# Kernel optimization log

Measured on AMD Instinct MI355X. Metric: run time of the kernel, lower is better.

The kernel has to match this reference:

```python
import jax, jax.numpy as jnp
import numpy as np

N_NODES = 100000
N_EDGES = 1600000
IN_DIM, HID_DIM, OUT_DIM = 128, 128, 64


def setup_inputs() -> dict:
    key = jax.random.key(0)
    k1, k2, k3, k4, k5 = jax.random.split(key, 5)
    x = jax.random.normal(k1, (N_NODES, IN_DIM), dtype=jnp.float32)
    edge_index = jax.random.randint(k2, (2, N_EDGES), 0, N_NODES, dtype=jnp.int64)
    # PyG GCNConv linear weights (no bias); Glorot-ish scale for stability
    W1 = jax.random.normal(k3, (IN_DIM, HID_DIM), dtype=jnp.float32) * 0.05
    W2 = jax.random.normal(k4, (HID_DIM, HID_DIM), dtype=jnp.float32) * 0.05
    W3 = jax.random.normal(k5, (HID_DIM, OUT_DIM), dtype=jnp.float32) * 0.05
    return {"x": x, "edge_index": edge_index, "W1": W1, "W2": W2, "W3": W3}


def _gcn_conv(h, W, src, dst, num_nodes):
    # GCNConv(add_self_loops=False, normalize=False, bias=False):
    # linear transform, then scatter-add messages from src into dst
    msg = jnp.take(h @ W, src, axis=0)          # [E, d_out] gather
    return jax.ops.segment_sum(msg, dst, num_segments=num_nodes)  # [N, d_out]


def reference(x, edge_index, W1, W2, W3):
    num_nodes = x.shape[0]
    src, dst = edge_index[0], edge_index[1]
    h = jax.nn.relu(_gcn_conv(x, W1, src, dst, num_nodes))
    # dropout p=0.0 / eval mode -> identity
    h = jax.nn.relu(_gcn_conv(h, W2, src, dst, num_nodes))
    out = _gcn_conv(h, W3, src, dst, num_nodes)
    return jax.nn.log_softmax(out, axis=1)
```

## Files before the change

kernel.cpp:

```cpp
#include <hip/hip_runtime.h>
#include <hip/hip_bf16.h>

#define KDIM 128

typedef __attribute__((ext_vector_type(8))) __bf16 bf16x8;
typedef __attribute__((ext_vector_type(4))) float f32x4;
typedef __attribute__((ext_vector_type(2))) float f32x2;

static __device__ __forceinline__ unsigned short f2bf(float f) {
  unsigned u = __float_as_uint(f);
  u += 0x7fffu + ((u >> 16) & 1u);
  return (unsigned short)(u >> 16);
}
static __device__ __forceinline__ unsigned pack_bf16x2(float a, float b) {
  return (unsigned)f2bf(a) | ((unsigned)f2bf(b) << 16);
}
static __device__ __forceinline__ unsigned relu2(unsigned u) {
  unsigned r = u;
  if (u & 0x00008000u) r &= 0xffff0000u;
  if (u & 0x80000000u) r &= 0x0000ffffu;
  return r;
}

static __device__ __forceinline__ unsigned char f2fp8(float f) {
#if __has_builtin(__builtin_amdgcn_cvt_pk_fp8_f32)
  return (unsigned char)(__builtin_amdgcn_cvt_pk_fp8_f32(f, f, 0, false) & 0xff);
#else
  unsigned s = (__float_as_uint(f) >> 24) & 0x80u;
  float a = fminf(fabsf(f), 448.f);
  if (a < 0.015625f) {
    unsigned m = (unsigned)(a * 512.f + 0.5f);
    return (unsigned char)(s | m);
  }
  unsigned v = __float_as_uint(a);
  v += 0x7ffffu + ((v >> 20) & 1u);
  unsigned em = (v >> 20) - 960u;
  if (em > 0x7eu) em = 0x7eu;
  return (unsigned char)(s | em);
#endif
}
static __device__ __forceinline__ float fp8dec(unsigned b) {
  unsigned s = (b & 0x80u) << 24;
  unsigned em = b & 0x7fu;
  float mag = (em >= 8) ? __uint_as_float((em + 960u) << 20)
                        : (float)em * 0.001953125f;
  return __uint_as_float(__float_as_uint(mag) | s);
}
static __device__ __forceinline__ float4 fp8x4_to_f32(unsigned u) {
#if __has_builtin(__builtin_amdgcn_cvt_pk_f32_fp8)
  f32x2 lo = __builtin_amdgcn_cvt_pk_f32_fp8(u, false);
  f32x2 hi = __builtin_amdgcn_cvt_pk_f32_fp8(u, true);
  return make_float4(lo[0], lo[1], hi[0], hi[1]);
#else
  return make_float4(fp8dec(u & 255u), fp8dec((u >> 8) & 255u),
                     fp8dec((u >> 16) & 255u), fp8dec(u >> 24));
#endif
}

__global__ __launch_bounds__(256) void wtrans_k(const float* __restrict__ W1,
                                                const float* __restrict__ W2,
                                                const float* __restrict__ W3,
                                                unsigned short* __restrict__ Wt) {
  const int t = blockIdx.x * 256 + threadIdx.x;
  if (t >= 40960) return;
  if (t < 16384) {
    Wt[t] = f2bf(W1[(t & 127) * 128 + (t >> 7)]);
  } else if (t < 32768) {
    const int u = t - 16384;
    Wt[t] = f2bf(W2[(u & 127) * 128 + (u >> 7)]);
  } else {
    const int u = t - 32768;
    Wt[t] = f2bf(W3[(u & 127) * 64 + (u >> 7)]);
  }
}

template<int NOUT, bool AF32, bool RELU>
__global__ __launch_bounds__(512) void gemm_mfma_k(const void* __restrict__ Av,
                                                   const unsigned short* __restrict__ Wt,
                                                   unsigned char* __restrict__ C, int M) {
  constexpr int NT = NOUT / 16;
  __shared__ unsigned short Ws[NOUT][136];

  const int tid = threadIdx.x;
  for (int i = tid; i < NOUT * 16; i += 512) {
    const int n = i >> 4, k8 = i & 15;
    const uint4 v = *reinterpret_cast<const uint4*>(&Wt[n * KDIM + k8 * 8]);
    *reinterpret_cast<uint4*>(&Ws[n][k8 * 8]) = v;
  }

  const int wv = tid >> 6;
  const int l  = tid & 63;
  const int am = l & 15;
  const int kb = l >> 4;
  const int arow_g = blockIdx.x * 128 + wv * 16 + am;
  const bool valid = arow_g < M;
  const int arow = valid ? arow_g : 0;

  uint4 afr[4];
  if constexpr (AF32) {
    const float* A = (const float*)Av;
    #pragma unroll
    for (int ks = 0; ks < 4; ++ks) {
      const float4 lo = *reinterpret_cast<const float4*>(&A[(size_t)arow * 128 + ks * 32 + kb * 8]);
      const float4 hi = *reinterpret_cast<const float4*>(&A[(size_t)arow * 128 + ks * 32 + kb * 8 + 4]);
      afr[ks] = make_uint4(pack_bf16x2(lo.x, lo.y), pack_bf16x2(lo.z, lo.w),
                           pack_bf16x2(hi.x, hi.y), pack_bf16x2(hi.z, hi.w));
    }
  } else {
    const unsigned* A = (const unsigned*)Av;
    #pragma unroll
    for (int ks = 0; ks < 4; ++ks) {
      uint4 u = *reinterpret_cast<const uint4*>(&A[(size_t)arow * 64 + ks * 16 + kb * 4]);
      if constexpr (RELU) {
        u.x = relu2(u.x); u.y = relu2(u.y); u.z = relu2(u.z); u.w = relu2(u.w);
      }
      afr[ks] = u;
    }
  }
  if (!valid) {
    afr[0] = make_uint4(0, 0, 0, 0); afr[1] = afr[0];
    afr[2] = afr[0];                 afr[3] = afr[0];
  }

  f32x4 acc[NT];
  #pragma unroll
  for (int nt = 0; nt < NT; ++nt) {
    acc[nt][0] = 0.f; acc[nt][1] = 0.f; acc[nt][2] = 0.f; acc[nt][3] = 0.f;
  }

  __syncthreads();
  #pragma unroll
  for (int ks = 0; ks < 4; ++ks) {
    const bf16x8 a = __builtin_bit_cast(bf16x8, afr[ks]);
    #pragma unroll
    for (int nt = 0; nt < NT; ++nt) {
      const uint4 bv = *reinterpret_cast<const uint4*>(&Ws[nt * 16 + am][ks * 32 + kb * 8]);
      acc[nt] = __builtin_amdgcn_mfma_f32_16x16x32_bf16(
          a, __builtin_bit_cast(bf16x8, bv), acc[nt], 0, 0, 0);
    }
  }

  const int crow0 = blockIdx.x * 128 + wv * 16 + kb * 4;
  #pragma unroll
  for (int nt = 0; nt < NT; ++nt) {
    #pragma unroll
    for (int r = 0; r < 4; ++r) {
      const int rr = crow0 + r;
      if (rr < M) C[(size_t)rr * NOUT + nt * 16 + am] = f2fp8(acc[nt][r]);
    }
  }
}

__global__ __launch_bounds__(512) void hist_k(const int* __restrict__ dst,
                                              int* __restrict__ histT,
                                              int E, int nbins) {
  __shared__ int h[512];
  for (int i = threadIdx.x; i < nbins; i += 512) h[i] = 0;
  __syncthreads();
  const int E4 = E >> 2;
  for (int i = blockIdx.x * 512 + threadIdx.x; i < E4; i += 256 * 512) {
    const int4 d4 = *reinterpret_cast<const int4*>(&dst[i * 4]);
    atomicAdd(&h[d4.x >> 8], 1);
    atomicAdd(&h[d4.y >> 8], 1);
    atomicAdd(&h[d4.z >> 8], 1);
    atomicAdd(&h[d4.w >> 8], 1);
  }
  if (blockIdx.x == 0 && threadIdx.x < (E & 3))
    atomicAdd(&h[dst[E4 * 4 + threadIdx.x] >> 8], 1);
  __syncthreads();
  for (int i = threadIdx.x; i < nbins; i += 512)
    histT[i * 256 + blockIdx.x] = h[i];
}

__global__ __launch_bounds__(256) void scan1_k(const int* __restrict__ in,
                                               int* __restrict__ out,
                                               int* __restrict__ bsum, int N) {
  __shared__ int ls[256];
  const int t = threadIdx.x;
  const int base = blockIdx.x * 2048 + t * 8;
  int v[8];
  if (base + 8 <= N) {
    *reinterpret_cast<int4*>(&v[0]) = *reinterpret_cast<const int4*>(&in[base]);
    *reinterpret_cast<int4*>(&v[4]) = *reinterpret_cast<const int4*>(&in[base + 4]);
  } else {
    #pragma unroll
    for (int j = 0; j < 8; ++j) v[j] = (base + j < N) ? in[base + j] : 0;
  }
  int s = 0;
  #pragma unroll
  for (int j = 0; j < 8; ++j) { const int tmp = v[j]; v[j] = s; s += tmp; }
  int x = s;
  ls[t] = x;
  __syncthreads();
  for (int off = 1; off < 256; off <<= 1) {
    int y = 0;
    if (t >= off) y = ls[t - off];
    __syncthreads();
    x += y;
    ls[t] = x;
    __syncthreads();
  }
  const int excl = x - s;
  #pragma unroll
  for (int j = 0; j < 8; ++j)
    if (base + j < N) out[base + j] = excl + v[j];
  if (t == 255) bsum[blockIdx.x] = x;
}

__global__ __launch_bounds__(64) void scan2_k(const int* __restrict__ bsum,
                                              int* __restrict__ bscan, int NB) {
  const int t = threadIdx.x;
  const int v = (t < NB) ? bsum[t] : 0;
  int x = v;
  #pragma unroll
  for (int off = 1; off < 64; off <<= 1) {
    const int y = __shfl_up(x, off, 64);
    if (t >= off) x += y;
  }
  bscan[t] = x - v;
}

__global__ __launch_bounds__(512) void binscatter_k(const int* __restrict__ src,
                                                    const int* __restrict__ dst,
                                                    const int* __restrict__ histOff,
                                                    const int* __restrict__ bscan,
                                                    unsigned* __restrict__ epack,
                                                    int E, int nbins) {
  __shared__ int cur[512];
  for (int i = threadIdx.x; i < nbins; i += 512) {
    const int gi = i * 256 + blockIdx.x;
    cur[i] = histOff[gi] + bscan[gi >> 11];
  }
  __syncthreads();
  const int E4 = E >> 2;
  for (int i = blockIdx.x * 512 + threadIdx.x; i < E4; i += 256 * 512) {
    const int4 d4 = *reinterpret_cast<const int4*>(&dst[i * 4]);
    const int4 s4 = *reinterpret_cast<const int4*>(&src[i * 4]);
    int p;
    p = atomicAdd(&cur[d4.x >> 8], 1); epack[p] = ((unsigned)(d4.x & 255) << 17) | (unsigned)s4.x;
    p = atomicAdd(&cur[d4.y >> 8], 1); epack[p] = ((unsigned)(d4.y & 255) << 17) | (unsigned)s4.y;
    p = atomicAdd(&cur[d4.z >> 8], 1); epack[p] = ((unsigned)(d4.z & 255) << 17) | (unsigned)s4.z;
    p = atomicAdd(&cur[d4.w >> 8], 1); epack[p] = ((unsigned)(d4.w & 255) << 17) | (unsigned)s4.w;
  }
  if (blockIdx.x == 0 && threadIdx.x < (E & 3)) {
    const int e = E4 * 4 + threadIdx.x;
    const int d = dst[e];
    const int p = atomicAdd(&cur[d >> 8], 1);
    epack[p] = ((unsigned)(d & 255) << 17) | (unsigned)src[e];
  }
}

__global__ __launch_bounds__(512) void binsort_k(const unsigned* __restrict__ epack,
                                                 const int* __restrict__ histOff,
                                                 const int* __restrict__ bscan,
                                                 int* __restrict__ rowptr,
                                                 int* __restrict__ col,
                                                 int N, int E, int nbins) {
  __shared__ int hist[256];
  __shared__ int ls[256];
  __shared__ int cur[256];
  const int b = blockIdx.x;
  const int t = threadIdx.x;
  const int i0 = b * 256;
  const int beg = histOff[i0] + bscan[i0 >> 11];
  int end = E;
  if (b + 1 < nbins) {
    const int i1 = (b + 1) * 256;
    end = histOff[i1] + bscan[i1 >> 11];
  }

  if (t < 256) hist[t] = 0;
  __syncthreads();
  for (int j = beg + t; j < end; j += 512)
    atomicAdd(&hist[epack[j] >> 17], 1);
  __syncthreads();

  int v = 0, x = 0;
  if (t < 256) { v = hist[t]; x = v; ls[t] = x; }
  __syncthreads();
  for (int off = 1; off < 256; off <<= 1) {
    int y = 0;
    if (t < 256 && t >= off) y = ls[t - off];
    __syncthreads();
    if (t < 256) { x += y; ls[t] = x; }
    __syncthreads();
  }
  if (t < 256) {
    const int excl = x - v;
    cur[t] = excl;
    const int g = b * 256 + t;
    if (g <= N) rowptr[g] = beg + excl;
  }
  if (b == nbins - 1 && t == 0) rowptr[N] = E;
  __syncthreads();
  for (int j = beg + t; j < end; j += 512) {
    const unsigned p = epack[j];
    const int pos = atomicAdd(&cur[p >> 17], 1);
    col[beg + pos] = (int)(p & 0x1ffffu);
  }
}

__global__ __launch_bounds__(256) void gather128_k(const uint2* __restrict__ H64,
                                                   const int* __restrict__ rowptr,
                                                   const int* __restrict__ col,
                                                   unsigned* __restrict__ out, int N) {
  const int w = (int)((blockIdx.x * 256u + threadIdx.x) >> 6);
  const int lane = threadIdx.x & 63;
  const int q = lane >> 4;
  const int l4 = lane & 15;
  if (w >= N) return;
  const int beg = __builtin_amdgcn_readfirstlane(rowptr[w]);
  const int end = __builtin_amdgcn_readfirstlane(rowptr[w + 1]);

  float4 a0A = make_float4(0.f, 0.f, 0.f, 0.f), a0B = make_float4(0.f, 0.f, 0.f, 0.f);
  float4 a1A = make_float4(0.f, 0.f, 0.f, 0.f), a1B = make_float4(0.f, 0.f, 0.f, 0.f);

  int e = beg;
  for (; e + 16 <= end; e += 16) {
    const int s0 = col[e + q];
    const int s1 = col[e + 4 + q];
    const int s2 = col[e + 8 + q];
    const int s3 = col[e + 12 + q];
    const uint2 u0 = H64[(size_t)s0 * 16 + l4];
    const uint2 u1 = H64[(size_t)s1 * 16 + l4];
    const uint2 u2 = H64[(size_t)s2 * 16 + l4];
    const uint2 u3 = H64[(size_t)s3 * 16 + l4];
    float4 v;
    v = fp8x4_to_f32(u0.x); a0A.x += v.x; a0A.y += v.y; a0A.z += v.z; a0A.w += v.w;
    v = fp8x4_to_f32(u0.y); a0B.x += v.x; a0B.y += v.y; a0B.z += v.z; a0B.w += v.w;
    v = fp8x4_to_f32(u1.x); a1A.x += v.x; a1A.y += v.y; a1A.z += v.z; a1A.w += v.w;
    v = fp8x4_to_f32(u1.y); a1B.x += v.x; a1B.y += v.y; a1B.z += v.z; a1B.w += v.w;
    v = fp8x4_to_f32(u2.x); a0A.x += v.x; a0A.y += v.y; a0A.z += v.z; a0A.w += v.w;
    v = fp8x4_to_f32(u2.y); a0B.x += v.x; a0B.y += v.y; a0B.z += v.z; a0B.w += v.w;
    v = fp8x4_to_f32(u3.x); a1A.x += v.x; a1A.y += v.y; a1A.z += v.z; a1A.w += v.w;
    v = fp8x4_to_f32(u3.y); a1B.x += v.x; a1B.y += v.y; a1B.z += v.z; a1B.w += v.w;
  }
  for (; e + 4 <= end; e += 4) {
    const uint2 u = H64[(size_t)col[e + q] * 16 + l4];
    float4 v;
    v = fp8x4_to_f32(u.x); a0A.x += v.x; a0A.y += v.y; a0A.z += v.z; a0A.w += v.w;
    v = fp8x4_to_f32(u.y); a0B.x += v.x; a0B.y += v.y; a0B.z += v.z; a0B.w += v.w;
  }
  if (q < end - e) {
    const uint2 u = H64[(size_t)col[e + q] * 16 + l4];
    float4 v;
    v = fp8x4_to_f32(u.x); a1A.x += v.x; a1A.y += v.y; a1A.z += v.z; a1A.w += v.w;
    v = fp8x4_to_f32(u.y); a1B.x += v.x; a1B.y += v.y; a1B.z += v.z; a1B.w += v.w;
  }

  float4 aA, aB;
  aA.x = a0A.x + a1A.x; aA.y = a0A.y + a1A.y;
  aA.z = a0A.z + a1A.z; aA.w = a0A.w + a1A.w;
  aB.x = a0B.x + a1B.x; aB.y = a0B.y + a1B.y;
  aB.z = a0B.z + a1B.z; aB.w = a0B.w + a1B.w;

  aA.x += __shfl_xor(aA.x, 16, 64); aA.x += __shfl_xor(aA.x, 32, 64);
  aA.y += __shfl_xor(aA.y, 16, 64); aA.y += __shfl_xor(aA.y, 32, 64);
  aA.z += __shfl_xor(aA.z, 16, 64); aA.z += __shfl_xor(aA.z, 32, 64);
  aA.w += __shfl_xor(aA.w, 16, 64); aA.w += __shfl_xor(aA.w, 32, 64);
  aB.x += __shfl_xor(aB.x, 16, 64); aB.x += __shfl_xor(aB.x, 32, 64);
  aB.y += __shfl_xor(aB.y, 16, 64); aB.y += __shfl_xor(aB.y, 32, 64);
  aB.z += __shfl_xor(aB.z, 16, 64); aB.z += __shfl_xor(aB.z, 32, 64);
  aB.w += __shfl_xor(aB.w, 16, 64); aB.w += __shfl_xor(aB.w, 32, 64);

  if (q == 0) {
    const uint4 pk = make_uint4(pack_bf16x2(aA.x, aA.y), pack_bf16x2(aA.z, aA.w),
                                pack_bf16x2(aB.x, aB.y), pack_bf16x2(aB.z, aB.w));
    *reinterpret_cast<uint4*>(&out[(size_t)w * 64 + l4 * 4]) = pk;
  }
}

__global__ __launch_bounds__(256) void gather64lsm_k(const unsigned* __restrict__ H32,
                                                     const int* __restrict__ rowptr,
                                                     const int* __restrict__ col,
                                                     float* __restrict__ out, int N) {
  const int w = (int)((blockIdx.x * 256u + threadIdx.x) >> 6);
  const int lane = threadIdx.x & 63;
  const int q = lane >> 4;
  const int l4 = lane & 15;
  if (w >= N) return;
  const int beg = __builtin_amdgcn_readfirstlane(rowptr[w]);
  const int end = __builtin_amdgcn_readfirstlane(rowptr[w + 1]);

  float4 acc0 = make_float4(0.f, 0.f, 0.f, 0.f);
  float4 acc1 = make_float4(0.f, 0.f, 0.f, 0.f);

  int e = beg;
  for (; e + 16 <= end; e += 16) {
    const int s0 = col[e + q];
    const int s1 = col[e + 4 + q];
    const int s2 = col[e + 8 + q];
    const int s3 = col[e + 12 + q];
    const unsigned u0 = H32[(size_t)s0 * 16 + l4];
    const unsigned u1 = H32[(size_t)s1 * 16 + l4];
    const unsigned u2 = H32[(size_t)s2 * 16 + l4];
    const unsigned u3 = H32[(size_t)s3 * 16 + l4];
    float4 v;
    v = fp8x4_to_f32(u0); acc0.x += v.x; acc0.y += v.y; acc0.z += v.z; acc0.w += v.w;
    v = fp8x4_to_f32(u1); acc1.x += v.x; acc1.y += v.y; acc1.z += v.z; acc1.w += v.w;
    v = fp8x4_to_f32(u2); acc0.x += v.x; acc0.y += v.y; acc0.z += v.z; acc0.w += v.w;
    v = fp8x4_to_f32(u3); acc1.x += v.x; acc1.y += v.y; acc1.z += v.z; acc1.w += v.w;
  }
  for (; e + 8 <= end; e += 8) {
    const int s0 = col[e + q];
    const int s1 = col[e + 4 + q];
    const float4 v0 = fp8x4_to_f32(H32[(size_t)s0 * 16 + l4]);
    const float4 v1 = fp8x4_to_f32(H32[(size_t)s1 * 16 + l4]);
    acc0.x += v0.x; acc0.y += v0.y; acc0.z += v0.z; acc0.w += v0.w;
    acc1.x += v1.x; acc1.y += v1.y; acc1.z += v1.z; acc1.w += v1.w;
  }
  if (e + 4 <= end) {
    const float4 v = fp8x4_to_f32(H32[(size_t)col[e + q] * 16 + l4]);
    acc0.x += v.x; acc0.y += v.y; acc0.z += v.z; acc0.w += v.w;
    e += 4;
  }
  if (e + q < end) {
    const float4 v = fp8x4_to_f32(H32[(size_t)col[e + q] * 16 + l4]);
    acc1.x += v.x; acc1.y += v.y; acc1.z += v.z; acc1.w += v.w;
  }

  float4 a;
  a.x = acc0.x + acc1.x;
  a.y = acc0.y + acc1.y;
  a.z = acc0.z + acc1.z;
  a.w = acc0.w + acc1.w;
  a.x += __shfl_xor(a.x, 16, 64); a.x += __shfl_xor(a.x, 32, 64);
  a.y += __shfl_xor(a.y, 16, 64); a.y += __shfl_xor(a.y, 32, 64);
  a.z += __shfl_xor(a.z, 16, 64); a.z += __shfl_xor(a.z, 32, 64);
  a.w += __shfl_xor(a.w, 16, 64); a.w += __shfl_xor(a.w, 32, 64);

  float m = fmaxf(fmaxf(a.x, a.y), fmaxf(a.z, a.w));
  #pragma unroll
  for (int o = 8; o > 0; o >>= 1) m = fmaxf(m, __shfl_xor(m, o, 64));
  float s = __expf(a.x - m) + __expf(a.y - m) + __expf(a.z - m) + __expf(a.w - m);
  #pragma unroll
  for (int o = 8; o > 0; o >>= 1) s += __shfl_xor(s, o, 64);
  const float ls = __logf(s);

  if (lane < 16) {
    *reinterpret_cast<float4*>(&out[(size_t)w * 64 + l4 * 4]) =
        make_float4(a.x - m - ls, a.y - m - ls, a.z - m - ls, a.w - m - ls);
  }
}

extern "C" void kernel_launch(void* const* d_in, const int* in_sizes, int n_in,
                              void* d_out, int out_size, void* d_ws, size_t ws_size,
                              hipStream_t stream) {
  const float* x  = (const float*)d_in[0];
  const int*   ei = (const int*)d_in[1];
  const float* W1 = (const float*)d_in[2];
  const float* W2 = (const float*)d_in[3];
  const float* W3 = (const float*)d_in[4];
  float* out = (float*)d_out;

  const int N = in_sizes[0] / KDIM;
  const int E = in_sizes[1] / 2;
  const int* src = ei;
  const int* dst = ei + E;

  const int nbins = (N + 255) / 256;
  const int ncells = nbins * 256;
  const int scan_blocks = (ncells + 2047) / 2048;

  unsigned char* H = (unsigned char*)d_ws;
  unsigned* AGGp = (unsigned*)(H + (size_t)N * 128);
  unsigned short* Wt1 = (unsigned short*)(AGGp + (size_t)N * 64);
  unsigned short* Wt2 = Wt1 + 128 * 128;
  unsigned short* Wt3 = Wt2 + 128 * 128;
  int* col     = (int*)(Wt3 + 64 * 128);
  int* rowptr  = col + E;
  int* histT   = rowptr + (N + 8);
  int* histOff = histT + 131072;
  int* bsum2   = histOff + 131072;
  int* bscan2  = bsum2 + 64;
  unsigned* epack = (unsigned*)AGGp;

  wtrans_k<<<(40960 + 255) / 256, 256, 0, stream>>>(W1, W2, W3, Wt1);

  hist_k<<<256, 512, 0, stream>>>(dst, histT, E, nbins);
  scan1_k<<<scan_blocks, 256, 0, stream>>>(histT, histOff, bsum2, ncells);
  scan2_k<<<1, 64, 0, stream>>>(bsum2, bscan2, scan_blocks);
  binscatter_k<<<256, 512, 0, stream>>>(src, dst, histOff, bscan2, epack, E, nbins);
  binsort_k<<<nbins, 512, 0, stream>>>(epack, histOff, bscan2, rowptr, col, N, E, nbins);

  const int gemm_grid = (N + 127) / 128;
  const int gather_grid = (N + 3) / 4;

  gemm_mfma_k<128, true, false><<<gemm_grid, 512, 0, stream>>>(x, Wt1, H, N);
  gather128_k<<<gather_grid, 256, 0, stream>>>((const uint2*)H, rowptr, col, AGGp, N);

  gemm_mfma_k<128, false, true><<<gemm_grid, 512, 0, stream>>>(AGGp, Wt2, H, N);
  gather128_k<<<gather_grid, 256, 0, stream>>>((const uint2*)H, rowptr, col, AGGp, N);

  gemm_mfma_k<64, false, true><<<gemm_grid, 512, 0, stream>>>(AGGp, Wt3, H, N);
  gather64lsm_k<<<gather_grid, 256, 0, stream>>>((const unsigned*)H, rowptr, col, out, N);
}
```

Measured before the change: 216.1 us.

## Merge weight transpose into histogram and run layer-1 GEMM alongside binscatter

The weight transpose/bf16 conversion is folded into the histogram kernel, with 160 threads per block covering the 40960 weight elements. The first-layer GEMM and the edge binscatter are combined into one launch that splits blocks by index, since the two are independent. This removes two kernel launches and lets GEMM work overlap the atomic-heavy scatter. In exchange, both paths share one shared-memory allocation sized for the GEMM, which may limit occupancy for the scatter blocks.

```diff
diff --git a/kernel.cpp b/kernel.cpp
--- a/kernel.cpp
+++ b/kernel.cpp
@@ -57,30 +57,13 @@
 #endif
 }
 
-__global__ __launch_bounds__(256) void wtrans_k(const float* __restrict__ W1,
-                                                const float* __restrict__ W2,
-                                                const float* __restrict__ W3,
-                                                unsigned short* __restrict__ Wt) {
-  const int t = blockIdx.x * 256 + threadIdx.x;
-  if (t >= 40960) return;
-  if (t < 16384) {
-    Wt[t] = f2bf(W1[(t & 127) * 128 + (t >> 7)]);
-  } else if (t < 32768) {
-    const int u = t - 16384;
-    Wt[t] = f2bf(W2[(u & 127) * 128 + (u >> 7)]);
-  } else {
-    const int u = t - 32768;
-    Wt[t] = f2bf(W3[(u & 127) * 64 + (u >> 7)]);
-  }
-}
-
 template<int NOUT, bool AF32, bool RELU>
-__global__ __launch_bounds__(512) void gemm_mfma_k(const void* __restrict__ Av,
-                                                   const unsigned short* __restrict__ Wt,
-                                                   unsigned char* __restrict__ C, int M) {
+static __device__ __forceinline__ void gemm_body(const void* __restrict__ Av,
+                                                 const unsigned short* __restrict__ Wt,
+                                                 unsigned char* __restrict__ C, int M,
+                                                 int bx,
+                                                 unsigned short (*Ws)[136]) {
   constexpr int NT = NOUT / 16;
-  __shared__ unsigned short Ws[NOUT][136];
-
   const int tid = threadIdx.x;
   for (int i = tid; i < NOUT * 16; i += 512) {
     const int n = i >> 4, k8 = i & 15;
@@ -92,7 +75,7 @@
   const int l  = tid & 63;
   const int am = l & 15;
   const int kb = l >> 4;
-  const int arow_g = blockIdx.x * 128 + wv * 16 + am;
+  const int arow_g = bx * 128 + wv * 16 + am;
   const bool valid = arow_g < M;
   const int arow = valid ? arow_g : 0;
 
@@ -140,7 +123,7 @@
     }
   }
 
-  const int crow0 = blockIdx.x * 128 + wv * 16 + kb * 4;
+  const int crow0 = bx * 128 + wv * 16 + kb * 4;
   #pragma unroll
   for (int nt = 0; nt < NT; ++nt) {
     #pragma unroll
@@ -151,9 +134,82 @@
   }
 }
 
-__global__ __launch_bounds__(512) void hist_k(const int* __restrict__ dst,
-                                              int* __restrict__ histT,
-                                              int E, int nbins) {
+template<int NOUT, bool AF32, bool RELU>
+__global__ __launch_bounds__(512) void gemm_mfma_k(const void* __restrict__ Av,
+                                                   const unsigned short* __restrict__ Wt,
+                                                   unsigned char* __restrict__ C, int M) {
+  __shared__ unsigned short Ws[NOUT][136];
+  gemm_body<NOUT, AF32, RELU>(Av, Wt, C, M, blockIdx.x, Ws);
+}
+
+static __device__ __forceinline__ void binscatter_body(const int* __restrict__ src,
+                                                       const int* __restrict__ dst,
+                                                       const int* __restrict__ histOff,
+                                                       const int* __restrict__ bscan,
+                                                       unsigned* __restrict__ epack,
+                                                       int E, int nbins, int bid,
+                                                       int* cur) {
+  for (int i = threadIdx.x; i < nbins; i += 512) {
+    const int gi = i * 256 + bid;
+    cur[i] = histOff[gi] + bscan[gi >> 11];
+  }
+  __syncthreads();
+  const int E4 = E >> 2;
+  for (int i = bid * 512 + threadIdx.x; i < E4; i += 256 * 512) {
+    const int4 d4 = *reinterpret_cast<const int4*>(&dst[i * 4]);
+    const int4 s4 = *reinterpret_cast<const int4*>(&src[i * 4]);
+    int p;
+    p = atomicAdd(&cur[d4.x >> 8], 1); epack[p] = ((unsigned)(d4.x & 255) << 17) | (unsigned)s4.x;
+    p = atomicAdd(&cur[d4.y >> 8], 1); epack[p] = ((unsigned)(d4.y & 255) << 17) | (unsigned)s4.y;
+    p = atomicAdd(&cur[d4.z >> 8], 1); epack[p] = ((unsigned)(d4.z & 255) << 17) | (unsigned)s4.z;
+    p = atomicAdd(&cur[d4.w >> 8], 1); epack[p] = ((unsigned)(d4.w & 255) << 17) | (unsigned)s4.w;
+  }
+  if (bid == 0 && threadIdx.x < (E & 3)) {
+    const int e = E4 * 4 + threadIdx.x;
+    const int d = dst[e];
+    const int p = atomicAdd(&cur[d >> 8], 1);
+    epack[p] = ((unsigned)(d & 255) << 17) | (unsigned)src[e];
+  }
+}
+
+__global__ __launch_bounds__(512) void mega1_k(const float* __restrict__ x,
+                                               const unsigned short* __restrict__ Wt1,
+                                               unsigned char* __restrict__ H, int M,
+                                               const int* __restrict__ src,
+                                               const int* __restrict__ dst,
+                                               const int* __restrict__ histOff,
+                                               const int* __restrict__ bscan,
+                                               unsigned* __restrict__ epack,
+                                               int E, int nbins, int gemm_grid) {
+  __shared__ unsigned short Ws[128][136];
+  if ((int)blockIdx.x < gemm_grid) {
+    gemm_body<128, true, false>(x, Wt1, H, M, blockIdx.x, Ws);
+  } else {
+    binscatter_body(src, dst, histOff, bscan, epack, E, nbins,
+                    blockIdx.x - gemm_grid, (int*)&Ws[0][0]);
+  }
+}
+
+__global__ __launch_bounds__(512) void histw_k(const int* __restrict__ dst,
+                                               int* __restrict__ histT,
+                                               int E, int nbins,
+                                               const float* __restrict__ W1,
+                                               const float* __restrict__ W2,
+                                               const float* __restrict__ W3,
+                                               unsigned short* __restrict__ Wt) {
+  if (threadIdx.x < 160) {
+    const int t = blockIdx.x * 160 + threadIdx.x;
+    if (t < 16384) {
+      Wt[t] = f2bf(W1[(t & 127) * 128 + (t >> 7)]);
+    } else if (t < 32768) {
+      const int u = t - 16384;
+      Wt[t] = f2bf(W2[(u & 127) * 128 + (u >> 7)]);
+    } else if (t < 40960) {
+      const int u = t - 32768;
+      Wt[t] = f2bf(W3[(u & 127) * 64 + (u >> 7)]);
+    }
+  }
+
   __shared__ int h[512];
   for (int i = threadIdx.x; i < nbins; i += 512) h[i] = 0;
   __syncthreads();
@@ -218,36 +274,6 @@
     if (t >= off) x += y;
   }
   bscan[t] = x - v;
-}
-
-__global__ __launch_bounds__(512) void binscatter_k(const int* __restrict__ src,
-                                                    const int* __restrict__ dst,
-                                                    const int* __restrict__ histOff,
-                                                    const int* __restrict__ bscan,
-                                                    unsigned* __restrict__ epack,
-                                                    int E, int nbins) {
-  __shared__ int cur[512];
-  for (int i = threadIdx.x; i < nbins; i += 512) {
-    const int gi = i * 256 + blockIdx.x;
-    cur[i] = histOff[gi] + bscan[gi >> 11];
-  }
-  __syncthreads();
-  const int E4 = E >> 2;
-  for (int i = blockIdx.x * 512 + threadIdx.x; i < E4; i += 256 * 512) {
-    const int4 d4 = *reinterpret_cast<const int4*>(&dst[i * 4]);
-    const int4 s4 = *reinterpret_cast<const int4*>(&src[i * 4]);
-    int p;
-    p = atomicAdd(&cur[d4.x >> 8], 1); epack[p] = ((unsigned)(d4.x & 255) << 17) | (unsigned)s4.x;
-    p = atomicAdd(&cur[d4.y >> 8], 1); epack[p] = ((unsigned)(d4.y & 255) << 17) | (unsigned)s4.y;
-    p = atomicAdd(&cur[d4.z >> 8], 1); epack[p] = ((unsigned)(d4.z & 255) << 17) | (unsigned)s4.z;
-    p = atomicAdd(&cur[d4.w >> 8], 1); epack[p] = ((unsigned)(d4.w & 255) << 17) | (unsigned)s4.w;
-  }
-  if (blockIdx.x == 0 && threadIdx.x < (E & 3)) {
-    const int e = E4 * 4 + threadIdx.x;
-    const int d = dst[e];
-    const int p = atomicAdd(&cur[d >> 8], 1);
-    epack[p] = ((unsigned)(d & 255) << 17) | (unsigned)src[e];
-  }
 }
 
 __global__ __launch_bounds__(512) void binsort_k(const unsigned* __restrict__ epack,
@@ -475,18 +501,17 @@
   int* bscan2  = bsum2 + 64;
   unsigned* epack = (unsigned*)AGGp;
 
-  wtrans_k<<<(40960 + 255) / 256, 256, 0, stream>>>(W1, W2, W3, Wt1);
-
-  hist_k<<<256, 512, 0, stream>>>(dst, histT, E, nbins);
+  const int gemm_grid = (N + 127) / 128;
+  const int gather_grid = (N + 3) / 4;
+
+  histw_k<<<256, 512, 0, stream>>>(dst, histT, E, nbins, W1, W2, W3, Wt1);
   scan1_k<<<scan_blocks, 256, 0, stream>>>(histT, histOff, bsum2, ncells);
   scan2_k<<<1, 64, 0, stream>>>(bsum2, bscan2, scan_blocks);
-  binscatter_k<<<256, 512, 0, stream>>>(src, dst, histOff, bscan2, epack, E, nbins);
+  mega1_k<<<gemm_grid + 256, 512, 0, stream>>>(x, Wt1, H, N, src, dst,
+                                               histOff, bscan2, epack,
+                                               E, nbins, gemm_grid);
   binsort_k<<<nbins, 512, 0, stream>>>(epack, histOff, bscan2, rowptr, col, N, E, nbins);
 
-  const int gemm_grid = (N + 127) / 128;
-  const int gather_grid = (N + 3) / 4;
-
-  gemm_mfma_k<128, true, false><<<gemm_grid, 512, 0, stream>>>(x, Wt1, H, N);
   gather128_k<<<gather_grid, 256, 0, stream>>>((const uint2*)H, rowptr, col, AGGp, N);
 
   gemm_mfma_k<128, false, true><<<gemm_grid, 512, 0, stream>>>(AGGp, Wt2, H, N);
```

After: 209.5 us. 3.1% less time.
